# Kernel tuning notes

Measured on AMD Instinct MI355X. Metric: run time of the kernel, lower is better.

The kernel has to match this reference:

```python
import jax, jax.numpy as jnp
import numpy as np

N_NODES = 1024
IN_FEATURES = 512
N_HEADS = 4
N_HIDDEN = 32  # out_features (128) // n_heads (4)
NEG_SLOPE = 0.2


def setup_inputs() -> dict:
    key = jax.random.key(0)
    k1, k2, k3, k4, k5 = jax.random.split(key, 5)
    h = jax.random.normal(k1, (N_NODES, IN_FEATURES), dtype=jnp.float32)
    adj_mat = jax.random.randint(k2, (N_NODES, N_NODES, 1), 0, 2, dtype=jnp.int32)
    s = 1.0 / np.sqrt(IN_FEATURES)
    W_l = jax.random.uniform(k3, (IN_FEATURES, N_HEADS * N_HIDDEN), jnp.float32, -s, s)
    W_r = jax.random.uniform(k4, (IN_FEATURES, N_HEADS * N_HIDDEN), jnp.float32, -s, s)
    sa = 1.0 / np.sqrt(N_HIDDEN)
    attn_w = jax.random.uniform(k5, (N_HIDDEN,), jnp.float32, -sa, sa)
    return {"h": h, "adj_mat": adj_mat, "W_l": W_l, "W_r": W_r, "attn_w": attn_w}


def reference(h, adj_mat, W_l, W_r, attn_w):
    # GraphAttentionV2Layer forward (eval mode: dropout = identity)
    n = h.shape[0]
    g_l = (h @ W_l).reshape(n, N_HEADS, N_HIDDEN)  # source-side (j)
    g_r = (h @ W_r).reshape(n, N_HEADS, N_HIDDEN)  # dest-side (i)
    # g_sum[i, j, h, f] = g_l[j] + g_r[i]  (repeat / repeat_interleave semantics)
    g_sum = g_l[None, :, :, :] + g_r[:, None, :, :]  # [N, N, H, hid]
    act = jnp.where(g_sum >= 0, g_sum, NEG_SLOPE * g_sum)
    e = jnp.einsum('ijhf,f->ijh', act, attn_w)  # [N, N, H]
    mask = (adj_mat == 0)  # broadcasts [N, N, 1] -> [N, N, H]
    e = jnp.where(mask, -jnp.inf, e)
    a = jax.nn.softmax(e, axis=1)  # softmax over neighbors j
    h_prime = jnp.einsum('ijh,jhf->ihf', a, g_r)  # note: aggregates g_r, per source
    h_prime = h_prime.reshape(n, N_HEADS * N_HIDDEN)  # is_concat=True
    # not output layer -> ELU activation (output dropout is identity in eval)
    out = jnp.where(h_prime > 0, h_prime, jnp.expm1(h_prime))
    return out
```

## Files before the change

### kernel.cpp

```cpp
#include <hip/hip_runtime.h>
#include <math.h>

#define N_NODES 1024
#define IN_F 512
#define N_HEADS 4
#define N_HID 32
#define OUT_F 128
#define GF 256
#define NEG_SLOPE 0.2f

__global__ __launch_bounds__(256, 2) void gat_gemm(
    const float* __restrict__ hmat, const float* __restrict__ Wl,
    const float* __restrict__ Wr, float* __restrict__ gpart,
    float* __restrict__ den)
{
  const int b = blockIdx.x;
  if (b < 16) den[b * 256 + threadIdx.x] = 0.f;
  const int kc = b & 7, ct = (b >> 3) & 3, it = b >> 5;
  const int i0 = it * 64, k0 = kc * 64, cb0 = ct * 64;
  const float* __restrict__ W = (cb0 < 128) ? (Wl + cb0) : (Wr + (cb0 - 128));

  __shared__ float As[16][68];
  __shared__ float Bs[16][64];

  const int tx = threadIdx.x & 15, ty = threadIdx.x >> 4;
  const int ar = threadIdx.x >> 2, ak = (threadIdx.x & 3) * 4;
  const int bk = threadIdx.x >> 4, bc = (threadIdx.x & 15) * 4;

  float4 acc0 = {0.f, 0.f, 0.f, 0.f}, acc1 = acc0, acc2 = acc0, acc3 = acc0;

  float4 av = *(const float4*)(hmat + (size_t)(i0 + ar) * IN_F + k0 + ak);
  float4 bv = *(const float4*)(W + (size_t)(k0 + bk) * OUT_F + bc);

  for (int t = 0; t < 64; t += 16) {
    __syncthreads();
    As[ak + 0][ar] = av.x; As[ak + 1][ar] = av.y;
    As[ak + 2][ar] = av.z; As[ak + 3][ar] = av.w;
    *(float4*)&Bs[bk][bc] = bv;
    __syncthreads();
    if (t < 48) {
      av = *(const float4*)(hmat + (size_t)(i0 + ar) * IN_F + k0 + t + 16 + ak);
      bv = *(const float4*)(W + (size_t)(k0 + t + 16 + bk) * OUT_F + bc);
    }
#pragma unroll
    for (int k = 0; k < 16; ++k) {
      const float4 a  = *(const float4*)&As[k][ty * 4];
      const float4 bb = *(const float4*)&Bs[k][tx * 4];
      acc0.x = fmaf(a.x, bb.x, acc0.x); acc0.y = fmaf(a.x, bb.y, acc0.y);
      acc0.z = fmaf(a.x, bb.z, acc0.z); acc0.w = fmaf(a.x, bb.w, acc0.w);
      acc1.x = fmaf(a.y, bb.x, acc1.x); acc1.y = fmaf(a.y, bb.y, acc1.y);
      acc1.z = fmaf(a.y, bb.z, acc1.z); acc1.w = fmaf(a.y, bb.w, acc1.w);
      acc2.x = fmaf(a.z, bb.x, acc2.x); acc2.y = fmaf(a.z, bb.y, acc2.y);
      acc2.z = fmaf(a.z, bb.z, acc2.z); acc2.w = fmaf(a.z, bb.w, acc2.w);
      acc3.x = fmaf(a.w, bb.x, acc3.x); acc3.y = fmaf(a.w, bb.y, acc3.y);
      acc3.z = fmaf(a.w, bb.z, acc3.z); acc3.w = fmaf(a.w, bb.w, acc3.w);
    }
  }
  const size_t rbase = (size_t)kc * N_NODES + i0 + ty * 4;
  const int cc = cb0 + tx * 4;
  *(float4*)(gpart + (rbase + 0) * GF + cc) = acc0;
  *(float4*)(gpart + (rbase + 1) * GF + cc) = acc1;
  *(float4*)(gpart + (rbase + 2) * GF + cc) = acc2;
  *(float4*)(gpart + (rbase + 3) * GF + cc) = acc3;
}

__global__ __launch_bounds__(256) void gat_reduceW(
    const float4* __restrict__ gp, float4* __restrict__ g)
{
  const int idx = blockIdx.x * 256 + threadIdx.x;
  float4 s = gp[idx];
#pragma unroll
  for (int c = 1; c < 8; ++c) {
    const float4 v = gp[idx + c * 65536];
    s.x += v.x; s.y += v.y; s.z += v.z; s.w += v.w;
  }
  g[idx] = s;
}

__global__ __launch_bounds__(256) void gat_escore(
    const float* __restrict__ g, const float* __restrict__ attn_w,
    const int* __restrict__ adj, float* __restrict__ p, float* __restrict__ den)
{
  __shared__ float4 gls[32][33];
  const int i0 = blockIdx.x * 8;
  const int jb = blockIdx.y * 32;
  {
    const int row = threadIdx.x >> 3;
    const int f4b = threadIdx.x & 7;
#pragma unroll
    for (int q = 0; q < 4; ++q) {
      const int f4 = f4b + 8 * q;
      gls[row][f4] = *(const float4*)(g + (size_t)(jb + row) * GF + f4 * 4);
    }
  }
  const int jl = threadIdx.x & 31;
  const int hh = (threadIdx.x >> 5) & 3;
  const int is = threadIdx.x >> 7;
  const int ibase = i0 + is * 4;

  float4 gg[4][8];
#pragma unroll
  for (int ii = 0; ii < 4; ++ii)
#pragma unroll
    for (int f4 = 0; f4 < 8; ++f4)
      gg[ii][f4] = *(const float4*)(g + (size_t)(ibase + ii) * GF + 128 +
                                    hh * N_HID + f4 * 4);
  float aw[N_HID];
#pragma unroll
  for (int f = 0; f < N_HID; ++f) aw[f] = attn_w[f];
  __syncthreads();

  float acc[4] = {0.f, 0.f, 0.f, 0.f};
#pragma unroll
  for (int f4 = 0; f4 < 8; ++f4) {
    const float4 gv = gls[jl][hh * 8 + f4];
#pragma unroll
    for (int ii = 0; ii < 4; ++ii) {
      float s;
      s = gv.x + gg[ii][f4].x;
      acc[ii] = fmaf(fmaxf(s, NEG_SLOPE * s), aw[f4 * 4 + 0], acc[ii]);
      s = gv.y + gg[ii][f4].y;
      acc[ii] = fmaf(fmaxf(s, NEG_SLOPE * s), aw[f4 * 4 + 1], acc[ii]);
      s = gv.z + gg[ii][f4].z;
      acc[ii] = fmaf(fmaxf(s, NEG_SLOPE * s), aw[f4 * 4 + 2], acc[ii]);
      s = gv.w + gg[ii][f4].w;
      acc[ii] = fmaf(fmaxf(s, NEG_SLOPE * s), aw[f4 * 4 + 3], acc[ii]);
    }
  }

  const int j = jb + jl;
  float4 pv;
  float* pvp = &pv.x;
#pragma unroll
  for (int ii = 0; ii < 4; ++ii) {
    const int a = adj[(size_t)(ibase + ii) * N_NODES + j];
    pvp[ii] = a ? __expf(acc[ii]) : 0.f;
  }
  *(float4*)(p + ((size_t)hh * N_NODES + j) * N_NODES + ibase) = pv;

  float d0 = pv.x, d1 = pv.y, d2 = pv.z, d3 = pv.w;
#pragma unroll
  for (int m = 1; m < 32; m <<= 1) {
    d0 += __shfl_xor(d0, m);
    d1 += __shfl_xor(d1, m);
    d2 += __shfl_xor(d2, m);
    d3 += __shfl_xor(d3, m);
  }
  if (jl == 0) {
    atomicAdd(&den[hh * N_NODES + ibase + 0], d0);
    atomicAdd(&den[hh * N_NODES + ibase + 1], d1);
    atomicAdd(&den[hh * N_NODES + ibase + 2], d2);
    atomicAdd(&den[hh * N_NODES + ibase + 3], d3);
  }
}

__global__ __launch_bounds__(256, 2) void gat_aggr(
    const float* __restrict__ p, const float* __restrict__ g,
    float* __restrict__ hpart)
{
  const int b = blockIdx.x;
  const int jc = b & 7, hh = (b >> 3) & 3, it = b >> 5;
  const int i0 = it * 64, j0 = jc * 128;

  __shared__ float Ps[16][64];
  __shared__ float Gs[16][32];

  const int f2 = threadIdx.x & 15, ig = threadIdx.x >> 4;
  const int pj = threadIdx.x >> 4, pi = (threadIdx.x & 15) * 4;
  const int gj = threadIdx.x >> 3, gf = (threadIdx.x & 7) * 4;

  const float* __restrict__ pbase =
      p + (size_t)hh * N_NODES * N_NODES + i0 + pi;
  const float* __restrict__ gbase = g + 128 + hh * N_HID + gf;

  float a00 = 0.f, a01 = 0.f, a10 = 0.f, a11 = 0.f;
  float a20 = 0.f, a21 = 0.f, a30 = 0.f, a31 = 0.f;

  float4 pv = *(const float4*)(pbase + (size_t)(j0 + pj) * N_NODES);
  float4 gv = {0.f, 0.f, 0.f, 0.f};
  if (threadIdx.x < 128)
    gv = *(const float4*)(gbase + (size_t)(j0 + gj) * GF);

  for (int c = 0; c < 8; ++c) {
    __syncthreads();
    *(float4*)&Ps[pj][pi] = pv;
    if (threadIdx.x < 128) *(float4*)&Gs[gj][gf] = gv;
    __syncthreads();
    if (c < 7) {
      pv = *(const float4*)(pbase + (size_t)(j0 + (c + 1) * 16 + pj) * N_NODES);
      if (threadIdx.x < 128)
        gv = *(const float4*)(gbase + (size_t)(j0 + (c + 1) * 16 + gj) * GF);
    }
#pragma unroll
    for (int k = 0; k < 16; ++k) {
      const float4 pp = *(const float4*)&Ps[k][ig * 4];
      const float2 gg = *(const float2*)&Gs[k][f2 * 2];
      a00 = fmaf(pp.x, gg.x, a00); a01 = fmaf(pp.x, gg.y, a01);
      a10 = fmaf(pp.y, gg.x, a10); a11 = fmaf(pp.y, gg.y, a11);
      a20 = fmaf(pp.z, gg.x, a20); a21 = fmaf(pp.z, gg.y, a21);
      a30 = fmaf(pp.w, gg.x, a30); a31 = fmaf(pp.w, gg.y, a31);
    }
  }
  float* hp = hpart + ((size_t)jc * N_NODES + i0 + ig * 4) * OUT_F +
              hh * N_HID + f2 * 2;
  *(float2*)(hp + 0 * OUT_F) = make_float2(a00, a01);
  *(float2*)(hp + 1 * OUT_F) = make_float2(a10, a11);
  *(float2*)(hp + 2 * OUT_F) = make_float2(a20, a21);
  *(float2*)(hp + 3 * OUT_F) = make_float2(a30, a31);
}

__global__ __launch_bounds__(256) void gat_fin(
    const float* __restrict__ hpart, const float* __restrict__ den,
    float* __restrict__ outp)
{
  const int flat = blockIdx.x * 256 + threadIdx.x;
  const int i = flat >> 7, hf = flat & 127, hh = hf >> 5;
  float t[8];
#pragma unroll
  for (int c = 0; c < 8; ++c)
    t[c] = hpart[(size_t)c * (N_NODES * OUT_F) + flat];
  float s = ((t[0] + t[1]) + (t[2] + t[3])) + ((t[4] + t[5]) + (t[6] + t[7]));
  float v = s / den[hh * N_NODES + i];
  outp[flat] = v > 0.f ? v : expm1f(v);
}

extern "C" void kernel_launch(void* const* d_in, const int* in_sizes, int n_in,
                              void* d_out, int out_size, void* d_ws, size_t ws_size,
                              hipStream_t stream) {
  const float* hmat  = (const float*)d_in[0];
  const int*   adj   = (const int*)d_in[1];
  const float* Wl    = (const float*)d_in[2];
  const float* Wr    = (const float*)d_in[3];
  const float* attnw = (const float*)d_in[4];
  float* outp = (float*)d_out;

  char* ws = (char*)d_ws;
  float* gpart = (float*)(ws);
  float* g     = (float*)(ws + (8u << 20));
  float* den   = (float*)(ws + (9u << 20));
  float* p     = (float*)(ws + (10u << 20));
  float* hpart = (float*)(ws + (26u << 20));

  gat_gemm<<<512, 256, 0, stream>>>(hmat, Wl, Wr, gpart, den);
  gat_reduceW<<<256, 256, 0, stream>>>((const float4*)gpart, (float4*)g);
  gat_escore<<<dim3(128, 32), 256, 0, stream>>>(g, attnw, adj, p, den);
  gat_aggr<<<512, 256, 0, stream>>>(p, g, hpart);
  gat_fin<<<512, 256, 0, stream>>>(hpart, den, outp);
}
```

Baseline: 115.5 us.

## Fuse attention scoring with aggregation and split leaky-ReLU into linear plus abs terms

Merges the score kernel and the aggregation GEMM into one kernel. Each block computes exp scores for a tile of (i, j) pairs and accumulates p*g_r directly, so the 16 MB probability matrix is never written to or read back from global memory. Leaky ReLU is rewritten as 0.6*s + 0.4*|s|. The linear part becomes per-node scalars (abuf/bbuf) precomputed in the reduce kernel, which leaves only an abs-FMA per feature in the inner loop. This drops a launch and a large amount of memory traffic. The cost is higher per-thread register use and heavier inner-loop arithmetic for the aggregation, plus shuffle reductions across the four j-groups.

```diff
diff --git a/kernel.cpp b/kernel.cpp
--- a/kernel.cpp
+++ b/kernel.cpp
@@ -64,153 +64,170 @@
   *(float4*)(gpart + (rbase + 3) * GF + cc) = acc3;
 }
 
-__global__ __launch_bounds__(256) void gat_reduceW(
-    const float4* __restrict__ gp, float4* __restrict__ g)
-{
-  const int idx = blockIdx.x * 256 + threadIdx.x;
-  float4 s = gp[idx];
+__global__ __launch_bounds__(256) void gat_reduceWab(
+    const float* __restrict__ gpart, const float* __restrict__ attn_w,
+    float* __restrict__ g, float* __restrict__ abuf, float* __restrict__ bbuf)
+{
+  const int tid = threadIdx.x;
+  const int l = tid & 63, r = tid >> 6;
+  const int row = blockIdx.x * 4 + r;
+  const size_t o = (size_t)row * GF + l * 4;
+  float4 s = *(const float4*)(gpart + o);
 #pragma unroll
   for (int c = 1; c < 8; ++c) {
-    const float4 v = gp[idx + c * 65536];
+    const float4 v = *(const float4*)(gpart + (size_t)c * (N_NODES * GF) + o);
     s.x += v.x; s.y += v.y; s.z += v.z; s.w += v.w;
   }
-  g[idx] = s;
-}
-
-__global__ __launch_bounds__(256) void gat_escore(
-    const float* __restrict__ g, const float* __restrict__ attn_w,
-    const int* __restrict__ adj, float* __restrict__ p, float* __restrict__ den)
-{
-  __shared__ float4 gls[32][33];
-  const int i0 = blockIdx.x * 8;
-  const int jb = blockIdx.y * 32;
+  *(float4*)(g + o) = s;
+  const float4 a4 = *(const float4*)(attn_w + (l & 7) * 4);
+  float d = 0.6f * (s.x * a4.x + s.y * a4.y + s.z * a4.z + s.w * a4.w);
+  d += __shfl_xor(d, 1);
+  d += __shfl_xor(d, 2);
+  d += __shfl_xor(d, 4);
+  if ((l & 7) == 0) {
+    const int hq = l >> 3;
+    if (hq < 4) abuf[hq * N_NODES + row] = d;
+    else        bbuf[(hq - 4) * N_NODES + row] = d;
+  }
+}
+
+__global__ __launch_bounds__(256, 2) void gat_fused(
+    const float* __restrict__ g, const float* __restrict__ abuf,
+    const float* __restrict__ bbuf, const float* __restrict__ attn_w,
+    const int* __restrict__ adj, float* __restrict__ num_part,
+    float* __restrict__ den)
+{
+  __shared__ float4 gl_s[32 * 32];
+  __shared__ float4 gr_s[32 * 32];
+  __shared__ float as_[4 * 33];
+
+  const int b = blockIdx.x;
+  const int jc = b & 7, it = b >> 3;
+  const int i0 = it * 16, j0 = jc * 128;
+
+  const int tid = threadIdx.x;
+  const int jg = tid & 3, hh = (tid >> 2) & 3, il = tid >> 4;
+  const int i = i0 + il;
+
+  const int srow = tid >> 3, sf4 = tid & 7, sjg = srow >> 3;
+
+  float4 gr_i[8], c2[8];
+#pragma unroll
+  for (int f4 = 0; f4 < 8; ++f4) {
+    gr_i[f4] = *(const float4*)(g + (size_t)i * GF + 128 + hh * N_HID + f4 * 4);
+    const float4 a4 = *(const float4*)(attn_w + f4 * 4);
+    c2[f4] = make_float4(0.4f * a4.x, 0.4f * a4.y, 0.4f * a4.z, 0.4f * a4.w);
+  }
+  const float beta = bbuf[hh * N_NODES + i];
+
+  int slot[8], wslot[4];
+#pragma unroll
+  for (int f4 = 0; f4 < 8; ++f4) slot[f4] = hh * 8 + ((f4 + jg + 2 * hh) & 7);
+#pragma unroll
+  for (int q = 0; q < 4; ++q) wslot[q] = q * 8 + ((sf4 + sjg + 2 * q) & 7);
+
+  float4 pgl[4], pgr[4];
+  float pa = 0.f;
   {
-    const int row = threadIdx.x >> 3;
-    const int f4b = threadIdx.x & 7;
+    const float* gsrc = g + (size_t)(j0 + srow) * GF;
 #pragma unroll
     for (int q = 0; q < 4; ++q) {
-      const int f4 = f4b + 8 * q;
-      gls[row][f4] = *(const float4*)(g + (size_t)(jb + row) * GF + f4 * 4);
-    }
-  }
-  const int jl = threadIdx.x & 31;
-  const int hh = (threadIdx.x >> 5) & 3;
-  const int is = threadIdx.x >> 7;
-  const int ibase = i0 + is * 4;
-
-  float4 gg[4][8];
-#pragma unroll
-  for (int ii = 0; ii < 4; ++ii)
-#pragma unroll
-    for (int f4 = 0; f4 < 8; ++f4)
-      gg[ii][f4] = *(const float4*)(g + (size_t)(ibase + ii) * GF + 128 +
-                                    hh * N_HID + f4 * 4);
-  float aw[N_HID];
-#pragma unroll
-  for (int f = 0; f < N_HID; ++f) aw[f] = attn_w[f];
-  __syncthreads();
-
-  float acc[4] = {0.f, 0.f, 0.f, 0.f};
-#pragma unroll
-  for (int f4 = 0; f4 < 8; ++f4) {
-    const float4 gv = gls[jl][hh * 8 + f4];
-#pragma unroll
-    for (int ii = 0; ii < 4; ++ii) {
-      float s;
-      s = gv.x + gg[ii][f4].x;
-      acc[ii] = fmaf(fmaxf(s, NEG_SLOPE * s), aw[f4 * 4 + 0], acc[ii]);
-      s = gv.y + gg[ii][f4].y;
-      acc[ii] = fmaf(fmaxf(s, NEG_SLOPE * s), aw[f4 * 4 + 1], acc[ii]);
-      s = gv.z + gg[ii][f4].z;
-      acc[ii] = fmaf(fmaxf(s, NEG_SLOPE * s), aw[f4 * 4 + 2], acc[ii]);
-      s = gv.w + gg[ii][f4].w;
-      acc[ii] = fmaf(fmaxf(s, NEG_SLOPE * s), aw[f4 * 4 + 3], acc[ii]);
-    }
-  }
-
-  const int j = jb + jl;
-  float4 pv;
-  float* pvp = &pv.x;
-#pragma unroll
-  for (int ii = 0; ii < 4; ++ii) {
-    const int a = adj[(size_t)(ibase + ii) * N_NODES + j];
-    pvp[ii] = a ? __expf(acc[ii]) : 0.f;
-  }
-  *(float4*)(p + ((size_t)hh * N_NODES + j) * N_NODES + ibase) = pv;
-
-  float d0 = pv.x, d1 = pv.y, d2 = pv.z, d3 = pv.w;
-#pragma unroll
-  for (int m = 1; m < 32; m <<= 1) {
-    d0 += __shfl_xor(d0, m);
-    d1 += __shfl_xor(d1, m);
-    d2 += __shfl_xor(d2, m);
-    d3 += __shfl_xor(d3, m);
-  }
-  if (jl == 0) {
-    atomicAdd(&den[hh * N_NODES + ibase + 0], d0);
-    atomicAdd(&den[hh * N_NODES + ibase + 1], d1);
-    atomicAdd(&den[hh * N_NODES + ibase + 2], d2);
-    atomicAdd(&den[hh * N_NODES + ibase + 3], d3);
-  }
-}
-
-__global__ __launch_bounds__(256, 2) void gat_aggr(
-    const float* __restrict__ p, const float* __restrict__ g,
-    float* __restrict__ hpart)
-{
-  const int b = blockIdx.x;
-  const int jc = b & 7, hh = (b >> 3) & 3, it = b >> 5;
-  const int i0 = it * 64, j0 = jc * 128;
-
-  __shared__ float Ps[16][64];
-  __shared__ float Gs[16][32];
-
-  const int f2 = threadIdx.x & 15, ig = threadIdx.x >> 4;
-  const int pj = threadIdx.x >> 4, pi = (threadIdx.x & 15) * 4;
-  const int gj = threadIdx.x >> 3, gf = (threadIdx.x & 7) * 4;
-
-  const float* __restrict__ pbase =
-      p + (size_t)hh * N_NODES * N_NODES + i0 + pi;
-  const float* __restrict__ gbase = g + 128 + hh * N_HID + gf;
-
-  float a00 = 0.f, a01 = 0.f, a10 = 0.f, a11 = 0.f;
-  float a20 = 0.f, a21 = 0.f, a30 = 0.f, a31 = 0.f;
-
-  float4 pv = *(const float4*)(pbase + (size_t)(j0 + pj) * N_NODES);
-  float4 gv = {0.f, 0.f, 0.f, 0.f};
-  if (threadIdx.x < 128)
-    gv = *(const float4*)(gbase + (size_t)(j0 + gj) * GF);
-
-  for (int c = 0; c < 8; ++c) {
-    __syncthreads();
-    *(float4*)&Ps[pj][pi] = pv;
-    if (threadIdx.x < 128) *(float4*)&Gs[gj][gf] = gv;
-    __syncthreads();
-    if (c < 7) {
-      pv = *(const float4*)(pbase + (size_t)(j0 + (c + 1) * 16 + pj) * N_NODES);
-      if (threadIdx.x < 128)
-        gv = *(const float4*)(gbase + (size_t)(j0 + (c + 1) * 16 + gj) * GF);
-    }
-#pragma unroll
-    for (int k = 0; k < 16; ++k) {
-      const float4 pp = *(const float4*)&Ps[k][ig * 4];
-      const float2 gg = *(const float2*)&Gs[k][f2 * 2];
-      a00 = fmaf(pp.x, gg.x, a00); a01 = fmaf(pp.x, gg.y, a01);
-      a10 = fmaf(pp.y, gg.x, a10); a11 = fmaf(pp.y, gg.y, a11);
-      a20 = fmaf(pp.z, gg.x, a20); a21 = fmaf(pp.z, gg.y, a21);
-      a30 = fmaf(pp.w, gg.x, a30); a31 = fmaf(pp.w, gg.y, a31);
-    }
-  }
-  float* hp = hpart + ((size_t)jc * N_NODES + i0 + ig * 4) * OUT_F +
-              hh * N_HID + f2 * 2;
-  *(float2*)(hp + 0 * OUT_F) = make_float2(a00, a01);
-  *(float2*)(hp + 1 * OUT_F) = make_float2(a10, a11);
-  *(float2*)(hp + 2 * OUT_F) = make_float2(a20, a21);
-  *(float2*)(hp + 3 * OUT_F) = make_float2(a30, a31);
+      pgl[q] = *(const float4*)(gsrc + (sf4 + 8 * q) * 4);
+      pgr[q] = *(const float4*)(gsrc + 128 + (sf4 + 8 * q) * 4);
+    }
+    if (tid < 128) pa = abuf[(tid >> 5) * N_NODES + j0 + (tid & 31)];
+  }
+
+  float4 num4[8];
+#pragma unroll
+  for (int f4 = 0; f4 < 8; ++f4) num4[f4] = make_float4(0.f, 0.f, 0.f, 0.f);
+  float den_t = 0.f;
+
+  for (int t = 0; t < 4; ++t) {
+    __syncthreads();
+#pragma unroll
+    for (int q = 0; q < 4; ++q) {
+      gl_s[srow * 32 + wslot[q]] = pgl[q];
+      gr_s[srow * 32 + wslot[q]] = pgr[q];
+    }
+    if (tid < 128) as_[(tid >> 5) * 33 + (tid & 31)] = pa;
+    __syncthreads();
+    if (t < 3) {
+      const float* gs2 = g + (size_t)(j0 + (t + 1) * 32 + srow) * GF;
+#pragma unroll
+      for (int q = 0; q < 4; ++q) {
+        pgl[q] = *(const float4*)(gs2 + (sf4 + 8 * q) * 4);
+        pgr[q] = *(const float4*)(gs2 + 128 + (sf4 + 8 * q) * 4);
+      }
+      if (tid < 128) pa = abuf[(tid >> 5) * N_NODES + j0 + (t + 1) * 32 + (tid & 31)];
+    }
+    const int4 ad0 = *(const int4*)(adj + (size_t)i * N_NODES + j0 + t * 32 + jg * 8);
+    const int4 ad1 = *(const int4*)(adj + (size_t)i * N_NODES + j0 + t * 32 + jg * 8 + 4);
+    const int* adp0 = (const int*)&ad0;
+    const int* adp1 = (const int*)&ad1;
+
+#pragma unroll
+    for (int jj = 0; jj < 8; ++jj) {
+      const int jl = jg * 8 + jj;
+      const float4* glrow = &gl_s[jl * 32];
+      const float4* grrow = &gr_s[jl * 32];
+      float4 a0 = make_float4(0.f, 0.f, 0.f, 0.f), a1 = a0;
+#pragma unroll
+      for (int f4 = 0; f4 < 8; f4 += 2) {
+        const float4 v0 = glrow[slot[f4]];
+        const float4 v1 = glrow[slot[f4 + 1]];
+        float sx, sy, sz, sw;
+        sx = v0.x + gr_i[f4].x; sy = v0.y + gr_i[f4].y;
+        sz = v0.z + gr_i[f4].z; sw = v0.w + gr_i[f4].w;
+        a0.x = fmaf(c2[f4].x, __builtin_fabsf(sx), a0.x);
+        a0.y = fmaf(c2[f4].y, __builtin_fabsf(sy), a0.y);
+        a0.z = fmaf(c2[f4].z, __builtin_fabsf(sz), a0.z);
+        a0.w = fmaf(c2[f4].w, __builtin_fabsf(sw), a0.w);
+        sx = v1.x + gr_i[f4 + 1].x; sy = v1.y + gr_i[f4 + 1].y;
+        sz = v1.z + gr_i[f4 + 1].z; sw = v1.w + gr_i[f4 + 1].w;
+        a1.x = fmaf(c2[f4 + 1].x, __builtin_fabsf(sx), a1.x);
+        a1.y = fmaf(c2[f4 + 1].y, __builtin_fabsf(sy), a1.y);
+        a1.z = fmaf(c2[f4 + 1].z, __builtin_fabsf(sz), a1.z);
+        a1.w = fmaf(c2[f4 + 1].w, __builtin_fabsf(sw), a1.w);
+      }
+      float e = ((a0.x + a0.y) + (a0.z + a0.w)) + ((a1.x + a1.y) + (a1.z + a1.w));
+      e += as_[hh * 33 + jl] + beta;
+      float p = __expf(e);
+      const int am = (jj < 4) ? adp0[jj] : adp1[jj - 4];
+      p = am ? p : 0.f;
+      den_t += p;
+#pragma unroll
+      for (int f4 = 0; f4 < 8; ++f4) {
+        const float4 gv = grrow[slot[f4]];
+        num4[f4].x = fmaf(p, gv.x, num4[f4].x);
+        num4[f4].y = fmaf(p, gv.y, num4[f4].y);
+        num4[f4].z = fmaf(p, gv.z, num4[f4].z);
+        num4[f4].w = fmaf(p, gv.w, num4[f4].w);
+      }
+    }
+  }
+
+#pragma unroll
+  for (int m = 1; m < 4; m <<= 1) {
+    den_t += __shfl_xor(den_t, m);
+#pragma unroll
+    for (int f4 = 0; f4 < 8; ++f4) {
+      num4[f4].x += __shfl_xor(num4[f4].x, m);
+      num4[f4].y += __shfl_xor(num4[f4].y, m);
+      num4[f4].z += __shfl_xor(num4[f4].z, m);
+      num4[f4].w += __shfl_xor(num4[f4].w, m);
+    }
+  }
+  if (jg == 0) {
+    float* np = num_part + ((size_t)jc * N_NODES + i) * OUT_F + hh * N_HID;
+#pragma unroll
+    for (int f4 = 0; f4 < 8; ++f4) *(float4*)(np + f4 * 4) = num4[f4];
+    atomicAdd(&den[hh * N_NODES + i], den_t);
+  }
 }
 
 __global__ __launch_bounds__(256) void gat_fin(
-    const float* __restrict__ hpart, const float* __restrict__ den,
+    const float* __restrict__ num_part, const float* __restrict__ den,
     float* __restrict__ outp)
 {
   const int flat = blockIdx.x * 256 + threadIdx.x;
@@ -218,7 +235,7 @@
   float t[8];
 #pragma unroll
   for (int c = 0; c < 8; ++c)
-    t[c] = hpart[(size_t)c * (N_NODES * OUT_F) + flat];
+    t[c] = num_part[(size_t)c * (N_NODES * OUT_F) + flat];
   float s = ((t[0] + t[1]) + (t[2] + t[3])) + ((t[4] + t[5]) + (t[6] + t[7]));
   float v = s / den[hh * N_NODES + i];
   outp[flat] = v > 0.f ? v : expm1f(v);
@@ -238,12 +255,12 @@
   float* gpart = (float*)(ws);
   float* g     = (float*)(ws + (8u << 20));
   float* den   = (float*)(ws + (9u << 20));
-  float* p     = (float*)(ws + (10u << 20));
-  float* hpart = (float*)(ws + (26u << 20));
+  float* abuf  = (float*)(ws + (9u << 20) + (64u << 10));
+  float* bbuf  = (float*)(ws + (9u << 20) + (128u << 10));
+  float* npart = (float*)(ws + (10u << 20));
 
   gat_gemm<<<512, 256, 0, stream>>>(hmat, Wl, Wr, gpart, den);
-  gat_reduceW<<<256, 256, 0, stream>>>((const float4*)gpart, (float4*)g);
-  gat_escore<<<dim3(128, 32), 256, 0, stream>>>(g, attnw, adj, p, den);
-  gat_aggr<<<512, 256, 0, stream>>>(p, g, hpart);
-  gat_fin<<<512, 256, 0, stream>>>(hpart, den, outp);
-}
+  gat_reduceWab<<<256, 256, 0, stream>>>(gpart, attnw, g, abuf, bbuf);
+  gat_fused<<<512, 256, 0, stream>>>(g, abuf, bbuf, attnw, adj, npart, den);
+  gat_fin<<<512, 256, 0, stream>>>(npart, den, outp);
+}
```

Measured after the change: 126.3 us. +9.4%, slower.
